# Performance work log

Hardware: AMD Instinct MI355X
Metric: run time of the kernel (lower is better)

Reference implementation:

```python
import jax, jax.numpy as jnp
import numpy as np

NVIEW = 6
N = 6400        # nodes (hardcoded in source: torch.empty(6400, 6))
D = 2048        # input_dim
H = 512         # hidden_dim
C = 256         # common_dim
E = 204800      # edges per view (avg degree 32)


def spmm(h, src, dst, val):
    # sparse_adj @ h : gather source rows, scale by edge value, scatter-add to dst
    msg = val[:, None] * h[src]              # [E, F]
    return jax.ops.segment_sum(msg, dst, num_segments=N)


def setup_inputs() -> dict:
    key = jax.random.key(0)
    ks = jax.random.split(key, 12)
    x = jax.random.normal(ks[0], (NVIEW, N, D), dtype=jnp.float32)
    adj_src = jax.random.randint(ks[1], (NVIEW, E), 0, N, dtype=jnp.int32)
    adj_dst = jax.random.randint(ks[2], (NVIEW, E), 0, N, dtype=jnp.int32)
    # normalized-adjacency-like positive values, scaled ~1/degree to keep activations sane
    adj_val = jax.random.uniform(ks[3], (NVIEW, E), dtype=jnp.float32) / 32.0
    # glorot-ish scaling
    Wb = jax.random.normal(ks[4], (NVIEW, D, H), dtype=jnp.float32) / np.sqrt(D)
    Wo = jax.random.normal(ks[5], (NVIEW, H, H), dtype=jnp.float32) / np.sqrt(H)
    Wf = jax.random.normal(ks[6], (NVIEW, H, H), dtype=jnp.float32) / np.sqrt(H)
    Wc0 = jax.random.normal(ks[7], (D, C), dtype=jnp.float32) / np.sqrt(D)
    Wc1 = jax.random.normal(ks[8], (C, C), dtype=jnp.float32) / np.sqrt(C)
    Wc2 = jax.random.normal(ks[9], (C, C), dtype=jnp.float32) / np.sqrt(C)
    gate_w = jax.random.normal(ks[10], (NVIEW, NVIEW, H + C), dtype=jnp.float32) / np.sqrt(H + C)
    gate_b = jax.random.normal(ks[11], (NVIEW, NVIEW), dtype=jnp.float32) * 0.01
    return {"x": x, "adj_val": adj_val, "Wb": Wb, "Wo": Wo, "Wf": Wf,
            "Wc0": Wc0, "Wc1": Wc1, "Wc2": Wc2, "gate_w": gate_w, "gate_b": gate_b,
            "adj_src": adj_src, "adj_dst": adj_dst}


def reference(x, adj_val, Wb, Wo, Wf, Wc0, Wc1, Wc2, gate_w, gate_b, adj_src, adj_dst):
    zs = []
    for v in range(NVIEW):
        src, dst, val = adj_src[v], adj_dst[v], adj_val[v]
        # view-specific 3-layer GCN (relu, relu, identity)
        hidden = jax.nn.relu(spmm(x[v] @ Wb[v], src, dst, val))   # [N, H]
        mid    = jax.nn.relu(spmm(hidden @ Wo[v], src, dst, val)) # [N, H]
        final  = spmm(mid @ Wf[v], src, dst, val)                 # [N, H]
        z_v = (hidden + mid + final) / 3.0                        # layer_agg == 'mean'
        # shared common 3-layer GCN
        c = jax.nn.relu(spmm(x[v] @ Wc0, src, dst, val))          # [N, C]
        c = jax.nn.relu(spmm(c @ Wc1, src, dst, val))
        c = jax.nn.relu(spmm(c @ Wc2, src, dst, val))
        zs.append(jnp.concatenate([c, z_v], axis=1))              # [N, C+H]
    Z = jnp.stack(zs, axis=0)                                     # [V, N, C+H]
    # gate scores: score_k[:, i] = Linear_{k,i}(z_i)
    scores = jnp.einsum('inf,kif->kni', Z, gate_w) + gate_b[:, None, :]  # [V, N, V]
    scores = jax.nn.softmax(scores, axis=-1)
    z_global = jnp.einsum('kni,inf->knf', scores, Z)              # [V, N, C+H]
    return (z_global, Z)
```

## Files before the change

### kernel.cpp

```cpp
#include <hip/hip_runtime.h>
#include <hip/hip_bf16.h>

#define NVIEW 6
#define NN    6400
#define DD    2048
#define HH    512
#define CC    256
#define EE    204800
#define ZF    768

typedef __bf16 bf16x8 __attribute__((ext_vector_type(8)));
typedef __bf16 bf16x4 __attribute__((ext_vector_type(4)));
typedef float  f32x4  __attribute__((ext_vector_type(4)));

__device__ __forceinline__ float b2f(unsigned short u) {
  union { unsigned int i; float f; } c; c.i = ((unsigned int)u) << 16; return c.f;
}

__device__ __forceinline__ void glds16(const void* g, void* l) {
  __builtin_amdgcn_global_load_lds((const __attribute__((address_space(1))) void*)g,
                                   (__attribute__((address_space(3))) void*)l, 16, 0, 0);
}

__global__ void k_hist(const int* __restrict__ dst, int* __restrict__ hist) {
  int e = blockIdx.x * 256 + threadIdx.x;
  int v = blockIdx.y;
  if (e < EE) atomicAdd(&hist[v * NN + dst[(size_t)v * EE + e]], 1);
}

__global__ __launch_bounds__(1024) void k_scan(const int* __restrict__ hist,
                                               int* __restrict__ rp) {
  int v = blockIdx.x;
  const int* h = hist + v * NN;
  int* r = rp + v * (NN + 1);
  __shared__ int part[1024];
  int t = threadIdx.x;
  const int CH = 7;
  int base = t * CH;
  int loc[CH];
  int s = 0;
#pragma unroll
  for (int i = 0; i < CH; i++) {
    int idx = base + i;
    int val = (idx < NN) ? h[idx] : 0;
    loc[i] = s;
    s += val;
  }
  part[t] = s;
  __syncthreads();
  for (int off = 1; off < 1024; off <<= 1) {
    int x = (t >= off) ? part[t - off] : 0;
    __syncthreads();
    part[t] += x;
    __syncthreads();
  }
  int pre = (t == 0) ? 0 : part[t - 1];
#pragma unroll
  for (int i = 0; i < CH; i++) {
    int idx = base + i;
    if (idx < NN) r[idx] = pre + loc[i];
  }
  if (t == 1023) r[NN] = part[1023];
}

__global__ void k_cursor(const int* __restrict__ rp, int* __restrict__ cur) {
  int i = blockIdx.x * 256 + threadIdx.x;
  if (i < NVIEW * NN) {
    int v = i / NN, n = i - v * NN;
    cur[i] = rp[v * (NN + 1) + n];
  }
}

__global__ void k_scatter(const int* __restrict__ src, const int* __restrict__ dstA,
                          const float* __restrict__ val, int* __restrict__ cur,
                          int2* __restrict__ sedge) {
  int e = blockIdx.x * 256 + threadIdx.x;
  int v = blockIdx.y;
  if (e < EE) {
    size_t idx = (size_t)v * EE + e;
    int d = dstA[idx];
    int pos = atomicAdd(&cur[v * NN + d], 1);
    sedge[(size_t)v * EE + pos] = make_int2(src[idx], __float_as_int(val[idx]));
  }
}

__global__ __launch_bounds__(256) void k_cvt(const float* __restrict__ in,
                                             __bf16* __restrict__ out) {
  size_t i = (size_t)blockIdx.x * 256 + threadIdx.x;
  float4 q = ((const float4*)in)[i];
  bf16x4 o;
  o[0] = (__bf16)q.x; o[1] = (__bf16)q.y; o[2] = (__bf16)q.z; o[3] = (__bf16)q.w;
  *(bf16x4*)(out + i * 4) = o;
}

__global__ __launch_bounds__(256) void k_tw(const float* __restrict__ in,
                                            __bf16* __restrict__ out, int K, int N,
                                            size_t inSB, size_t outSB) {
  __shared__ float sh[32][33];
  int b = blockIdx.z;
  int k0 = blockIdx.x * 32, n0 = blockIdx.y * 32;
  int tx = threadIdx.x & 31, ty = threadIdx.x >> 5;
  const float* I = in + (size_t)b * inSB;
  __bf16* O = out + (size_t)b * outSB;
#pragma unroll
  for (int r = 0; r < 4; r++)
    sh[ty + r * 8][tx] = I[(size_t)(k0 + ty + r * 8) * N + n0 + tx];
  __syncthreads();
#pragma unroll
  for (int r = 0; r < 4; r++)
    O[(size_t)(n0 + ty + r * 8) * K + k0 + tx] = (__bf16)sh[tx][ty + r * 8];
}

__global__ __launch_bounds__(512, 2) void k_g256(
    const __bf16* __restrict__ A, const __bf16* __restrict__ BT,
    __bf16* __restrict__ C, int K, int Nc, int nbn, int bpv, int wPerView)
{
  __shared__ __bf16 ldsv[65536];
  int tid = threadIdx.x, lane = tid & 63, w = tid >> 6;

  int nwg = gridDim.x;
  int q8 = nwg >> 3, r8 = nwg & 7;
  int orig = blockIdx.x;
  int xcd = orig & 7, j = orig >> 3;
  int swz = (xcd < r8 ? xcd * (q8 + 1) : r8 * (q8 + 1) + (xcd - r8) * q8) + j;
  int v = swz / bpv; int rr = swz - v * bpv;
  int bm = rr / nbn; int bn = rr - bm * nbn;

  const __bf16* Av = A + (size_t)v * NN * K + (size_t)(bm * 256) * K;
  const __bf16* Bv = BT + (wPerView ? (size_t)v * Nc * K : 0) + (size_t)(bn * 256) * K;

  f32x4 acc[8][4];
#pragma unroll
  for (int m = 0; m < 8; m++)
#pragma unroll
    for (int n = 0; n < 4; n++) acc[m][n] = (f32x4){0.f, 0.f, 0.f, 0.f};

  const int wr = (w >> 2) * 128, wc = (w & 3) * 64;
  const int gq = lane >> 4, l15 = lane & 15;

#define STAGE_UNIT(Gp, LOFF, KH, KT)                                          \
  {                                                                           \
    _Pragma("unroll")                                                         \
    for (int g2 = 0; g2 < 2; g2++) {                                          \
      int chunk = (KH) * 1024 + (w + g2 * 8) * 64 + lane;                     \
      int row_ = chunk & 255, kkg_ = chunk >> 8;                              \
      glds16(Gp + (size_t)row_ * K + (KT) * 64 + kkg_ * 8,                    \
             ldsv + (LOFF) + chunk * 8);                                      \
    }                                                                         \
  }

#define PH_READS(KK, MH, LOADB)                                               \
  {                                                                           \
    _Pragma("unroll")                                                         \
    for (int m = 0; m < 4; m++)                                               \
      aF[m] = *(const bf16x8*)&Ab[(((KK) * 4 + gq) * 256 + wr + (MH) * 64 +   \
                                   m * 16 + l15) * 8];                        \
    if (LOADB) {                                                              \
      _Pragma("unroll")                                                       \
      for (int n = 0; n < 4; n++)                                             \
        bF[n] = *(const bf16x8*)&Bb[(((KK) * 4 + gq) * 256 + wc + n * 16 +    \
                                     l15) * 8];                               \
    }                                                                         \
  }

#define PH_MFMA(MH)                                                           \
  {                                                                           \
    __builtin_amdgcn_s_barrier();                                             \
    asm volatile("s_waitcnt lgkmcnt(0)" ::: "memory");                        \
    __builtin_amdgcn_sched_barrier(0);                                        \
    __builtin_amdgcn_s_setprio(1);                                            \
    _Pragma("unroll")                                                         \
    for (int m = 0; m < 4; m++)                                               \
      _Pragma("unroll")                                                       \
      for (int n = 0; n < 4; n++)                                             \
        acc[(MH) * 4 + m][n] = __builtin_amdgcn_mfma_f32_16x16x32_bf16(       \
            aF[m], bF[n], acc[(MH) * 4 + m][n], 0, 0, 0);                     \
    __builtin_amdgcn_s_setprio(0);                                            \
    __builtin_amdgcn_s_barrier();                                             \
  }

  const int nt = K >> 6;
  const int ni = nt >> 1;

  STAGE_UNIT(Av, 0,     0, 0);
  STAGE_UNIT(Bv, 16384, 0, 0);
  STAGE_UNIT(Av, 0,     1, 0);
  STAGE_UNIT(Bv, 16384, 1, 0);
  STAGE_UNIT(Av, 32768, 0, 1);
  STAGE_UNIT(Bv, 49152, 0, 1);
  asm volatile("s_waitcnt vmcnt(4)" ::: "memory");
  __builtin_amdgcn_s_barrier();

  bf16x8 aF[4], bF[4];
  for (int i = 0; i < ni; ++i) {
    int t1 = 2 * i + 1, t2 = 2 * i + 2, t3 = 2 * i + 3;
    bool more = (i + 1 < ni);
    const __bf16* Ab = ldsv;
    const __bf16* Bb = ldsv + 16384;
    PH_READS(0, 0, true);  STAGE_UNIT(Av, 32768, 1, t1);              PH_MFMA(0);
    PH_READS(0, 1, false); STAGE_UNIT(Bv, 49152, 1, t1);              PH_MFMA(1);
    PH_READS(1, 0, true);  if (more) STAGE_UNIT(Av, 0,     0, t2);    PH_MFMA(0);
    PH_READS(1, 1, false); if (more) STAGE_UNIT(Bv, 16384, 0, t2);
    if (more) asm volatile("s_waitcnt vmcnt(4)" ::: "memory");
    else      asm volatile("s_waitcnt vmcnt(0)" ::: "memory");
    PH_MFMA(1);
    Ab = ldsv + 32768; Bb = ldsv + 49152;
    PH_READS(0, 0, true);  if (more) STAGE_UNIT(Av, 0,     1, t2);    PH_MFMA(0);
    PH_READS(0, 1, false); if (more) STAGE_UNIT(Bv, 16384, 1, t2);    PH_MFMA(1);
    PH_READS(1, 0, true);  if (more) STAGE_UNIT(Av, 32768, 0, t3);    PH_MFMA(0);
    PH_READS(1, 1, false);
    if (more) {
      STAGE_UNIT(Bv, 49152, 0, t3);
      asm volatile("s_waitcnt vmcnt(4)" ::: "memory");
    }
    PH_MFMA(1);
  }

#undef STAGE_UNIT
#undef PH_READS
#undef PH_MFMA

  __bf16* Cv = C + (size_t)v * NN * Nc;
#pragma unroll
  for (int m = 0; m < 8; m++) {
    int rbase = bm * 256 + wr + m * 16 + (lane >> 4) * 4;
#pragma unroll
    for (int q = 0; q < 4; q++) {
      __bf16* cp = Cv + (size_t)(rbase + q) * Nc + bn * 256 + wc + l15;
#pragma unroll
      for (int n = 0; n < 4; n++) cp[n * 16] = (__bf16)acc[m][n][q];
    }
  }
}

template <int LDIN, int FOFF, int F, int CHUNKS, int MODE>
__global__ __launch_bounds__(256) void k_spmm(
    const __bf16* __restrict__ in, const int* __restrict__ rp,
    const int2* __restrict__ sedge, void* __restrict__ out,
    const __bf16* __restrict__ h1, const __bf16* __restrict__ h2)
{
  int id = blockIdx.x;
  int s = id & 7, j = id >> 3;
  int ch, v, rowblk;
  if (CHUNKS == 2) {
    ch = s >> 2; int q = s & 3;
    v = j / 400; int t = j - v * 400;
    rowblk = t * 4 + q;
  } else {
    ch = 0;
    v = j / 200; int t = j - v * 200;
    rowblk = t * 8 + s;
  }
  int wid = threadIdx.x >> 6, lane = threadIdx.x & 63;
  int n = rowblk * 4 + wid;
  int f0 = ch * 256 + lane * 4;

  const int* rpv = rp + v * (NN + 1);
  int e = rpv[n], end = rpv[n + 1];
  const int2* ev = sedge + (size_t)v * EE;
  const __bf16* inv = in + (size_t)v * NN * LDIN + FOFF;

  float a0 = 0.f, a1 = 0.f, a2 = 0.f, a3 = 0.f;
  for (; e + 4 <= end; e += 4) {
    int2 e0 = ev[e], e1 = ev[e + 1], e2 = ev[e + 2], e3 = ev[e + 3];
    float w0 = __int_as_float(e0.y), w1 = __int_as_float(e1.y);
    float w2 = __int_as_float(e2.y), w3 = __int_as_float(e3.y);
    ushort4 r0 = *(const ushort4*)(inv + (size_t)e0.x * LDIN + f0);
    ushort4 r1 = *(const ushort4*)(inv + (size_t)e1.x * LDIN + f0);
    ushort4 r2 = *(const ushort4*)(inv + (size_t)e2.x * LDIN + f0);
    ushort4 r3 = *(const ushort4*)(inv + (size_t)e3.x * LDIN + f0);
    a0 += w0 * b2f(r0.x); a1 += w0 * b2f(r0.y); a2 += w0 * b2f(r0.z); a3 += w0 * b2f(r0.w);
    a0 += w1 * b2f(r1.x); a1 += w1 * b2f(r1.y); a2 += w1 * b2f(r1.z); a3 += w1 * b2f(r1.w);
    a0 += w2 * b2f(r2.x); a1 += w2 * b2f(r2.y); a2 += w2 * b2f(r2.z); a3 += w2 * b2f(r2.w);
    a0 += w3 * b2f(r3.x); a1 += w3 * b2f(r3.y); a2 += w3 * b2f(r3.z); a3 += w3 * b2f(r3.w);
  }
  if (e + 2 <= end) {
    int2 e0 = ev[e], e1 = ev[e + 1];
    float w0 = __int_as_float(e0.y), w1 = __int_as_float(e1.y);
    ushort4 r0 = *(const ushort4*)(inv + (size_t)e0.x * LDIN + f0);
    ushort4 r1 = *(const ushort4*)(inv + (size_t)e1.x * LDIN + f0);
    a0 += w0 * b2f(r0.x); a1 += w0 * b2f(r0.y); a2 += w0 * b2f(r0.z); a3 += w0 * b2f(r0.w);
    a0 += w1 * b2f(r1.x); a1 += w1 * b2f(r1.y); a2 += w1 * b2f(r1.z); a3 += w1 * b2f(r1.w);
    e += 2;
  }
  if (e < end) {
    int2 e0 = ev[e];
    float w0 = __int_as_float(e0.y);
    ushort4 r0 = *(const ushort4*)(inv + (size_t)e0.x * LDIN + f0);
    a0 += w0 * b2f(r0.x); a1 += w0 * b2f(r0.y); a2 += w0 * b2f(r0.z); a3 += w0 * b2f(r0.w);
  }

  if (MODE == 0) {
    __bf16* o = (__bf16*)out + ((size_t)v * NN + n) * F + f0;
    bf16x4 ov;
    ov[0] = (__bf16)fmaxf(a0, 0.f); ov[1] = (__bf16)fmaxf(a1, 0.f);
    ov[2] = (__bf16)fmaxf(a2, 0.f); ov[3] = (__bf16)fmaxf(a3, 0.f);
    *(bf16x4*)o = ov;
  } else if (MODE == 1) {
    float* o = (float*)out + ((size_t)v * NN + n) * ZF + f0;
    o[0] = fmaxf(a0, 0.f); o[1] = fmaxf(a1, 0.f);
    o[2] = fmaxf(a2, 0.f); o[3] = fmaxf(a3, 0.f);
  } else {
    const __bf16* hh = h1 + ((size_t)v * NN + n) * 512 + f0;
    const __bf16* mm = h2 + ((size_t)v * NN + n) * 512 + f0;
    ushort4 hu = *(const ushort4*)hh;
    ushort4 mu = *(const ushort4*)mm;
    float* o = (float*)out + ((size_t)v * NN + n) * ZF + CC + f0;
    o[0] = (b2f(hu.x) + b2f(mu.x) + a0) * (1.f / 3.f);
    o[1] = (b2f(hu.y) + b2f(mu.y) + a1) * (1.f / 3.f);
    o[2] = (b2f(hu.z) + b2f(mu.z) + a2) * (1.f / 3.f);
    o[3] = (b2f(hu.w) + b2f(mu.w) + a3) * (1.f / 3.f);
  }
}

__global__ __launch_bounds__(256) void k_gate(
    const float* __restrict__ Z, const float* __restrict__ gw,
    const float* __restrict__ gb, float* __restrict__ zg)
{
  __shared__ float Zl[NVIEW * ZF];
  __shared__ float sred[36];
  __shared__ float pl[36];
  int n = blockIdx.x, tid = threadIdx.x;

  for (int idx = tid; idx < NVIEW * ZF; idx += 256) {
    int i = idx / ZF, f = idx - i * ZF;
    Zl[idx] = Z[((size_t)i * NN + n) * ZF + f];
  }
  if (tid < 36) sred[tid] = 0.f;
  __syncthreads();

  float acc[36];
#pragma unroll
  for (int p = 0; p < 36; p++) acc[p] = 0.f;
#pragma unroll
  for (int q = 0; q < 3; q++) {
    int f = tid + q * 256;
    float zv[NVIEW];
#pragma unroll
    for (int i = 0; i < NVIEW; i++) zv[i] = Zl[i * ZF + f];
#pragma unroll
    for (int k = 0; k < NVIEW; k++)
#pragma unroll
      for (int i = 0; i < NVIEW; i++)
        acc[k * 6 + i] += zv[i] * gw[(k * 6 + i) * ZF + f];
  }
  int lane = tid & 63;
#pragma unroll
  for (int p = 0; p < 36; p++) {
    float x = acc[p];
    x += __shfl_down(x, 32, 64);
    x += __shfl_down(x, 16, 64);
    x += __shfl_down(x, 8, 64);
    x += __shfl_down(x, 4, 64);
    x += __shfl_down(x, 2, 64);
    x += __shfl_down(x, 1, 64);
    if (lane == 0) atomicAdd(&sred[p], x);
  }
  __syncthreads();

  if (tid < NVIEW) {
    int k = tid;
    float sc[NVIEW];
    float mx = -1e30f;
#pragma unroll
    for (int i = 0; i < NVIEW; i++) {
      sc[i] = sred[k * 6 + i] + gb[k * 6 + i];
      mx = fmaxf(mx, sc[i]);
    }
    float sum = 0.f;
#pragma unroll
    for (int i = 0; i < NVIEW; i++) { sc[i] = __expf(sc[i] - mx); sum += sc[i]; }
    float inv = 1.f / sum;
#pragma unroll
    for (int i = 0; i < NVIEW; i++) pl[k * 6 + i] = sc[i] * inv;
  }
  __syncthreads();

#pragma unroll
  for (int q = 0; q < 3; q++) {
    int f = tid + q * 256;
    float zv[NVIEW];
#pragma unroll
    for (int i = 0; i < NVIEW; i++) zv[i] = Zl[i * ZF + f];
#pragma unroll
    for (int k = 0; k < NVIEW; k++) {
      float o = 0.f;
#pragma unroll
      for (int i = 0; i < NVIEW; i++) o += pl[k * 6 + i] * zv[i];
      zg[((size_t)k * NN + n) * ZF + f] = o;
    }
  }
}

extern "C" void kernel_launch(void* const* d_in, const int* in_sizes, int n_in,
                              void* d_out, int out_size, void* d_ws, size_t ws_size,
                              hipStream_t stream) {
  const float* x    = (const float*)d_in[0];
  const float* aval = (const float*)d_in[1];
  const float* Wb   = (const float*)d_in[2];
  const float* Wo   = (const float*)d_in[3];
  const float* Wf   = (const float*)d_in[4];
  const float* Wc0  = (const float*)d_in[5];
  const float* Wc1  = (const float*)d_in[6];
  const float* Wc2  = (const float*)d_in[7];
  const float* gw   = (const float*)d_in[8];
  const float* gb   = (const float*)d_in[9];
  const int*   asrc = (const int*)d_in[10];
  const int*   adst = (const int*)d_in[11];

  float* zg = (float*)d_out;
  float* Z  = zg + (size_t)NVIEW * NN * ZF;
  __bf16* xb = (__bf16*)d_out;

  char* w = (char*)d_ws;
  auto alloc = [&](size_t bytes) {
    char* p = w;
    w += (bytes + 255) & ~(size_t)255;
    return p;
  };
  int*    hist  = (int*)alloc((size_t)NVIEW * NN * 4);
  int*    rp    = (int*)alloc((size_t)NVIEW * (NN + 1) * 4);
  int2*   sedge = (int2*)alloc((size_t)NVIEW * EE * 8);
  __bf16* Wfu   = (__bf16*)alloc((size_t)NVIEW * ZF * DD * 2);
  __bf16* WoT   = (__bf16*)alloc((size_t)NVIEW * HH * HH * 2);
  __bf16* WfT   = (__bf16*)alloc((size_t)NVIEW * HH * HH * 2);
  __bf16* Wc1T  = (__bf16*)alloc((size_t)CC * CC * 2);
  __bf16* Wc2T  = (__bf16*)alloc((size_t)CC * CC * 2);
  __bf16* tf768 = (__bf16*)alloc((size_t)NVIEW * NN * ZF * 2);
  __bf16* t512b = (__bf16*)alloc((size_t)NVIEW * NN * HH * 2);
  __bf16* hidb  = (__bf16*)alloc((size_t)NVIEW * NN * HH * 2);
  __bf16* midb  = (__bf16*)alloc((size_t)NVIEW * NN * HH * 2);
  __bf16* tcb   = (__bf16*)alloc((size_t)NVIEW * NN * CC * 2);
  __bf16* cbb   = (__bf16*)alloc((size_t)NVIEW * NN * CC * 2);

  (void)hipMemsetAsync(hist, 0, (size_t)NVIEW * NN * 4, stream);
  k_hist<<<dim3(800, NVIEW), 256, 0, stream>>>(adst, hist);
  k_scan<<<NVIEW, 1024, 0, stream>>>(hist, rp);
  k_cursor<<<150, 256, 0, stream>>>(rp, hist);
  k_scatter<<<dim3(800, NVIEW), 256, 0, stream>>>(asrc, adst, aval, hist, sedge);

  k_cvt<<<76800, 256, 0, stream>>>(x, xb);
  k_tw<<<dim3(64, 16, NVIEW), 256, 0, stream>>>(Wb, Wfu, DD, HH,
                                                (size_t)DD * HH, (size_t)ZF * DD);
  k_tw<<<dim3(64, 8, NVIEW), 256, 0, stream>>>(Wc0, Wfu + (size_t)HH * DD, DD, CC,
                                               0, (size_t)ZF * DD);
  k_tw<<<dim3(16, 16, NVIEW), 256, 0, stream>>>(Wo, WoT, HH, HH,
                                                (size_t)HH * HH, (size_t)HH * HH);
  k_tw<<<dim3(16, 16, NVIEW), 256, 0, stream>>>(Wf, WfT, HH, HH,
                                                (size_t)HH * HH, (size_t)HH * HH);
  k_tw<<<dim3(8, 8, 1), 256, 0, stream>>>(Wc1, Wc1T, CC, CC, 0, 0);
  k_tw<<<dim3(8, 8, 1), 256, 0, stream>>>(Wc2, Wc2T, CC, CC, 0, 0);

  k_g256<<<450, 512, 0, stream>>>(xb, Wfu, tf768, DD, ZF, 3, 75, 1);
  k_spmm<768, 0, 512, 2, 0><<<19200, 256, 0, stream>>>(tf768, rp, sedge, hidb, nullptr, nullptr);
  k_spmm<768, 512, 256, 1, 0><<<9600, 256, 0, stream>>>(tf768, rp, sedge, cbb, nullptr, nullptr);

  k_g256<<<300, 512, 0, stream>>>(hidb, WoT, t512b, HH, HH, 2, 50, 1);
  k_spmm<512, 0, 512, 2, 0><<<19200, 256, 0, stream>>>(t512b, rp, sedge, midb, nullptr, nullptr);
  k_g256<<<150, 512, 0, stream>>>(cbb, Wc1T, tcb, CC, CC, 1, 25, 0);
  k_spmm<256, 0, 256, 1, 0><<<9600, 256, 0, stream>>>(tcb, rp, sedge, cbb, nullptr, nullptr);
  k_g256<<<300, 512, 0, stream>>>(midb, WfT, t512b, HH, HH, 2, 50, 1);
  k_spmm<512, 0, 512, 2, 2><<<19200, 256, 0, stream>>>(t512b, rp, sedge, Z, hidb, midb);
  k_g256<<<150, 512, 0, stream>>>(cbb, Wc2T, tcb, CC, CC, 1, 25, 0);
  k_spmm<256, 0, 256, 1, 1><<<9600, 256, 0, stream>>>(tcb, rp, sedge, Z, nullptr, nullptr);

  k_gate<<<NN, 256, 0, stream>>>(Z, gw, gb, zg);
}
```

Baseline: 1.246 ms.

## Double-buffer GEMM LDS fragment reads and widen SpMM gather unroll to 8

The GEMM main loop now keeps two register sets of A/B fragments. The next phase's LDS reads are issued between two halves of the current MFMA batch, so LDS latency overlaps matrix math and one barrier per phase is dropped. The vmcnt waits are re-tuned to match the reordered global-to-LDS staging. Separately, the SpMM gather loop is unrolled to 8 edges, with all index and row loads issued before accumulating, to get more memory-level parallelism. The extra fragment registers may raise VGPR pressure, and the reordered waits and barriers risk subtle race bugs.

```diff
diff --git a/kernel.cpp b/kernel.cpp
--- a/kernel.cpp
+++ b/kernel.cpp
@@ -138,6 +138,8 @@
   const int wr = (w >> 2) * 128, wc = (w & 3) * 64;
   const int gq = lane >> 4, l15 = lane & 15;
 
+  bf16x8 aFr[2][4], bFr[2][4];
+
 #define STAGE_UNIT(Gp, LOFF, KH, KT)                                          \
   {                                                                           \
     _Pragma("unroll")                                                         \
@@ -149,34 +151,39 @@
     }                                                                         \
   }
 
-#define PH_READS(KK, MH, LOADB)                                               \
+#define RD_A(SET, BUFO, KK, MH)                                               \
   {                                                                           \
     _Pragma("unroll")                                                         \
     for (int m = 0; m < 4; m++)                                               \
-      aF[m] = *(const bf16x8*)&Ab[(((KK) * 4 + gq) * 256 + wr + (MH) * 64 +   \
-                                   m * 16 + l15) * 8];                        \
-    if (LOADB) {                                                              \
+      aFr[SET][m] = *(const bf16x8*)&ldsv[(BUFO) +                            \
+          (((KK) * 4 + gq) * 256 + wr + (MH) * 64 + m * 16 + l15) * 8];       \
+  }
+
+#define RD_B(SET, BUFO, KK)                                                   \
+  {                                                                           \
+    _Pragma("unroll")                                                         \
+    for (int n = 0; n < 4; n++)                                               \
+      bFr[SET][n] = *(const bf16x8*)&ldsv[(BUFO) + 16384 +                    \
+          (((KK) * 4 + gq) * 256 + wc + n * 16 + l15) * 8];                   \
+  }
+
+#define MFMA_HALF(ASET, BSET, MH, M0)                                         \
+  {                                                                           \
+    __builtin_amdgcn_s_setprio(1);                                            \
+    _Pragma("unroll")                                                         \
+    for (int m = (M0); m < (M0) + 2; m++)                                     \
       _Pragma("unroll")                                                       \
       for (int n = 0; n < 4; n++)                                             \
-        bF[n] = *(const bf16x8*)&Bb[(((KK) * 4 + gq) * 256 + wc + n * 16 +    \
-                                     l15) * 8];                               \
-    }                                                                         \
-  }
-
-#define PH_MFMA(MH)                                                           \
+        acc[(MH) * 4 + m][n] = __builtin_amdgcn_mfma_f32_16x16x32_bf16(       \
+            aFr[ASET][m], bFr[BSET][n], acc[(MH) * 4 + m][n], 0, 0, 0);       \
+    __builtin_amdgcn_s_setprio(0);                                            \
+  }
+
+#define PH_TOP()                                                              \
   {                                                                           \
     __builtin_amdgcn_s_barrier();                                             \
     asm volatile("s_waitcnt lgkmcnt(0)" ::: "memory");                        \
     __builtin_amdgcn_sched_barrier(0);                                        \
-    __builtin_amdgcn_s_setprio(1);                                            \
-    _Pragma("unroll")                                                         \
-    for (int m = 0; m < 4; m++)                                               \
-      _Pragma("unroll")                                                       \
-      for (int n = 0; n < 4; n++)                                             \
-        acc[(MH) * 4 + m][n] = __builtin_amdgcn_mfma_f32_16x16x32_bf16(       \
-            aF[m], bF[n], acc[(MH) * 4 + m][n], 0, 0, 0);                     \
-    __builtin_amdgcn_s_setprio(0);                                            \
-    __builtin_amdgcn_s_barrier();                                             \
   }
 
   const int nt = K >> 6;
@@ -190,35 +197,74 @@
   STAGE_UNIT(Bv, 49152, 0, 1);
   asm volatile("s_waitcnt vmcnt(4)" ::: "memory");
   __builtin_amdgcn_s_barrier();
-
-  bf16x8 aF[4], bF[4];
+  RD_A(1, 0, 0, 0); RD_B(0, 0, 0);
+
   for (int i = 0; i < ni; ++i) {
     int t1 = 2 * i + 1, t2 = 2 * i + 2, t3 = 2 * i + 3;
     bool more = (i + 1 < ni);
-    const __bf16* Ab = ldsv;
-    const __bf16* Bb = ldsv + 16384;
-    PH_READS(0, 0, true);  STAGE_UNIT(Av, 32768, 1, t1);              PH_MFMA(0);
-    PH_READS(0, 1, false); STAGE_UNIT(Bv, 49152, 1, t1);              PH_MFMA(1);
-    PH_READS(1, 0, true);  if (more) STAGE_UNIT(Av, 0,     0, t2);    PH_MFMA(0);
-    PH_READS(1, 1, false); if (more) STAGE_UNIT(Bv, 16384, 0, t2);
-    if (more) asm volatile("s_waitcnt vmcnt(4)" ::: "memory");
-    else      asm volatile("s_waitcnt vmcnt(0)" ::: "memory");
-    PH_MFMA(1);
-    Ab = ldsv + 32768; Bb = ldsv + 49152;
-    PH_READS(0, 0, true);  if (more) STAGE_UNIT(Av, 0,     1, t2);    PH_MFMA(0);
-    PH_READS(0, 1, false); if (more) STAGE_UNIT(Bv, 16384, 1, t2);    PH_MFMA(1);
-    PH_READS(1, 0, true);  if (more) STAGE_UNIT(Av, 32768, 0, t3);    PH_MFMA(0);
-    PH_READS(1, 1, false);
+    PH_TOP();
+    MFMA_HALF(1, 0, 0, 0);
+    RD_A(0, 0, 0, 1);
+    STAGE_UNIT(Av, 32768, 1, t1);
+    asm volatile("s_waitcnt vmcnt(6)" ::: "memory");
+    MFMA_HALF(1, 0, 0, 2);
+    PH_TOP();
+    MFMA_HALF(0, 0, 1, 0);
+    RD_A(1, 0, 1, 0); RD_B(1, 0, 1);
+    STAGE_UNIT(Bv, 49152, 1, t1);
+    MFMA_HALF(0, 0, 1, 2);
+    PH_TOP();
+    MFMA_HALF(1, 1, 0, 0);
+    RD_A(0, 0, 1, 1);
     if (more) {
+      STAGE_UNIT(Av, 0, 0, t2);
+      asm volatile("s_waitcnt vmcnt(6)" ::: "memory");
+    } else {
+      asm volatile("s_waitcnt vmcnt(4)" ::: "memory");
+    }
+    MFMA_HALF(1, 1, 0, 2);
+    PH_TOP();
+    MFMA_HALF(0, 1, 1, 0);
+    RD_A(1, 32768, 0, 0); RD_B(0, 32768, 0);
+    if (more) STAGE_UNIT(Bv, 16384, 0, t2);
+    MFMA_HALF(0, 1, 1, 2);
+    PH_TOP();
+    MFMA_HALF(1, 0, 0, 0);
+    RD_A(0, 32768, 0, 1);
+    if (more) {
+      STAGE_UNIT(Av, 0, 1, t2);
+      asm volatile("s_waitcnt vmcnt(6)" ::: "memory");
+    } else {
+      asm volatile("s_waitcnt vmcnt(0)" ::: "memory");
+    }
+    MFMA_HALF(1, 0, 0, 2);
+    PH_TOP();
+    MFMA_HALF(0, 0, 1, 0);
+    RD_A(1, 32768, 1, 0); RD_B(1, 32768, 1);
+    if (more) STAGE_UNIT(Bv, 16384, 1, t2);
+    MFMA_HALF(0, 0, 1, 2);
+    PH_TOP();
+    MFMA_HALF(1, 1, 0, 0);
+    RD_A(0, 32768, 1, 1);
+    if (more) {
+      STAGE_UNIT(Av, 32768, 0, t3);
+      asm volatile("s_waitcnt vmcnt(6)" ::: "memory");
+    }
+    MFMA_HALF(1, 1, 0, 2);
+    PH_TOP();
+    MFMA_HALF(0, 1, 1, 0);
+    if (more) {
+      RD_A(1, 0, 0, 0); RD_B(0, 0, 0);
       STAGE_UNIT(Bv, 49152, 0, t3);
-      asm volatile("s_waitcnt vmcnt(4)" ::: "memory");
-    }
-    PH_MFMA(1);
+    }
+    MFMA_HALF(0, 1, 1, 2);
   }
 
 #undef STAGE_UNIT
-#undef PH_READS
-#undef PH_MFMA
+#undef RD_A
+#undef RD_B
+#undef MFMA_HALF
+#undef PH_TOP
 
   __bf16* Cv = C + (size_t)v * NN * Nc;
 #pragma unroll
@@ -261,33 +307,41 @@
   const __bf16* inv = in + (size_t)v * NN * LDIN + FOFF;
 
   float a0 = 0.f, a1 = 0.f, a2 = 0.f, a3 = 0.f;
-  for (; e + 4 <= end; e += 4) {
-    int2 e0 = ev[e], e1 = ev[e + 1], e2 = ev[e + 2], e3 = ev[e + 3];
-    float w0 = __int_as_float(e0.y), w1 = __int_as_float(e1.y);
-    float w2 = __int_as_float(e2.y), w3 = __int_as_float(e3.y);
-    ushort4 r0 = *(const ushort4*)(inv + (size_t)e0.x * LDIN + f0);
-    ushort4 r1 = *(const ushort4*)(inv + (size_t)e1.x * LDIN + f0);
-    ushort4 r2 = *(const ushort4*)(inv + (size_t)e2.x * LDIN + f0);
-    ushort4 r3 = *(const ushort4*)(inv + (size_t)e3.x * LDIN + f0);
-    a0 += w0 * b2f(r0.x); a1 += w0 * b2f(r0.y); a2 += w0 * b2f(r0.z); a3 += w0 * b2f(r0.w);
-    a0 += w1 * b2f(r1.x); a1 += w1 * b2f(r1.y); a2 += w1 * b2f(r1.z); a3 += w1 * b2f(r1.w);
-    a0 += w2 * b2f(r2.x); a1 += w2 * b2f(r2.y); a2 += w2 * b2f(r2.z); a3 += w2 * b2f(r2.w);
-    a0 += w3 * b2f(r3.x); a1 += w3 * b2f(r3.y); a2 += w3 * b2f(r3.z); a3 += w3 * b2f(r3.w);
-  }
-  if (e + 2 <= end) {
-    int2 e0 = ev[e], e1 = ev[e + 1];
-    float w0 = __int_as_float(e0.y), w1 = __int_as_float(e1.y);
-    ushort4 r0 = *(const ushort4*)(inv + (size_t)e0.x * LDIN + f0);
-    ushort4 r1 = *(const ushort4*)(inv + (size_t)e1.x * LDIN + f0);
-    a0 += w0 * b2f(r0.x); a1 += w0 * b2f(r0.y); a2 += w0 * b2f(r0.z); a3 += w0 * b2f(r0.w);
-    a0 += w1 * b2f(r1.x); a1 += w1 * b2f(r1.y); a2 += w1 * b2f(r1.z); a3 += w1 * b2f(r1.w);
-    e += 2;
-  }
-  if (e < end) {
+  for (; e + 8 <= end; e += 8) {
+    int2 ee[8]; ushort4 rrv[8];
+#pragma unroll
+    for (int u = 0; u < 8; u++) ee[u] = ev[e + u];
+#pragma unroll
+    for (int u = 0; u < 8; u++)
+      rrv[u] = *(const ushort4*)(inv + (size_t)ee[u].x * LDIN + f0);
+#pragma unroll
+    for (int u = 0; u < 8; u++) {
+      float wv = __int_as_float(ee[u].y);
+      a0 += wv * b2f(rrv[u].x); a1 += wv * b2f(rrv[u].y);
+      a2 += wv * b2f(rrv[u].z); a3 += wv * b2f(rrv[u].w);
+    }
+  }
+  if (e + 4 <= end) {
+    int2 ee[4]; ushort4 rrv[4];
+#pragma unroll
+    for (int u = 0; u < 4; u++) ee[u] = ev[e + u];
+#pragma unroll
+    for (int u = 0; u < 4; u++)
+      rrv[u] = *(const ushort4*)(inv + (size_t)ee[u].x * LDIN + f0);
+#pragma unroll
+    for (int u = 0; u < 4; u++) {
+      float wv = __int_as_float(ee[u].y);
+      a0 += wv * b2f(rrv[u].x); a1 += wv * b2f(rrv[u].y);
+      a2 += wv * b2f(rrv[u].z); a3 += wv * b2f(rrv[u].w);
+    }
+    e += 4;
+  }
+  for (; e < end; ++e) {
     int2 e0 = ev[e];
     float w0 = __int_as_float(e0.y);
     ushort4 r0 = *(const ushort4*)(inv + (size_t)e0.x * LDIN + f0);
-    a0 += w0 * b2f(r0.x); a1 += w0 * b2f(r0.y); a2 += w0 * b2f(r0.z); a3 += w0 * b2f(r0.w);
+    a0 += w0 * b2f(r0.x); a1 += w0 * b2f(r0.y);
+    a2 += w0 * b2f(r0.z); a3 += w0 * b2f(r0.w);
   }
 
   if (MODE == 0) {
```

Result: slower. 1.356 ms (+8.8%).
